# Kernel optimization log

Measured on AMD Instinct MI355X. Metric: run time of the kernel, lower is better.

## Reference

```python
import jax, jax.numpy as jnp
import numpy as np

B, S, E, H = 1, 2048, 1024, 16
D = E // H  # head_dim = 64


def setup_inputs() -> dict:
    key = jax.random.key(0)
    ks = jax.random.split(key, 9)
    sd = 0.02
    hidden_states = jax.random.normal(ks[0], (B, S, E), dtype=jnp.float32)
    # causal mask: positions with mask==0 are filled with -inf (per masked_fill_)
    mask = jnp.tril(jnp.ones((1, 1, S, S), dtype=bool))
    Wq = jax.random.normal(ks[1], (E, E), dtype=jnp.float32) * sd
    bq = jax.random.normal(ks[2], (E,), dtype=jnp.float32) * sd
    Wk = jax.random.normal(ks[3], (D, E), dtype=jnp.float32) * sd
    bk = jax.random.normal(ks[4], (D,), dtype=jnp.float32) * sd
    Wv = jax.random.normal(ks[5], (D, E), dtype=jnp.float32) * sd
    bv = jax.random.normal(ks[6], (D,), dtype=jnp.float32) * sd
    Wo = jax.random.normal(ks[7], (E, E), dtype=jnp.float32) * sd
    bo = jax.random.normal(ks[8], (E,), dtype=jnp.float32) * sd
    return {"hidden_states": hidden_states, "mask": mask,
            "Wq": Wq, "bq": bq, "Wk": Wk, "bk": bk,
            "Wv": Wv, "bv": bv, "Wo": Wo, "bo": bo}


def reference(hidden_states, mask, Wq, bq, Wk, bk, Wv, bv, Wo, bo):
    bsz, tgt_len, embed_dim = hidden_states.shape
    # projections (torch Linear: x @ W^T + b)
    q = hidden_states @ Wq.T + bq                       # [B, S, E]
    q = q.reshape(bsz, tgt_len, H, D).transpose(0, 2, 1, 3)  # [B, H, S, D]
    k = hidden_states @ Wk.T + bk                       # [B, S, D] shared single KV head
    v = hidden_states @ Wv.T + bv                       # [B, S, D]
    scaling = jnp.sqrt(jnp.asarray(D, dtype=hidden_states.dtype))
    # QK^T with implicit broadcast of the shared K head (instead of expand)
    scores = jnp.einsum('bhqd,bkd->bhqk', q, k) / scaling   # [B, H, S, S]
    scores = jnp.where(mask, scores, -jnp.inf)
    probs = jax.nn.softmax(scores, axis=-1)             # dropout p=0 -> identity
    attn = jnp.einsum('bhqk,bkd->bhqd', probs, v)       # [B, H, S, D]
    attn = attn.transpose(0, 2, 1, 3).reshape(bsz, tgt_len, H * D)
    return attn @ Wo.T + bo                             # [B, S, E]
```

## Files before the change

kernel.cpp:

```cpp
#include <hip/hip_runtime.h>
#include <hip/hip_bf16.h>

typedef __hip_bfloat16 bf16;
typedef __attribute__((ext_vector_type(8))) short short8;
typedef __attribute__((ext_vector_type(4))) float f32x4;

__device__ __forceinline__ short8 ld8(const void* p) { return *(const short8*)p; }

__device__ __forceinline__ void async_cp16(bf16* lds, const bf16* g) {
    __builtin_amdgcn_global_load_lds(
        (const __attribute__((address_space(1))) unsigned int*)g,
        (__attribute__((address_space(3))) unsigned int*)lds, 16, 0, 0);
}

struct bf4 { bf16 a, b, c, d; };

__global__ void cast_kernel(const float* __restrict__ s0, bf16* __restrict__ d0, int n0_,
                            const float* __restrict__ s1, bf16* __restrict__ d1, int n1_,
                            const float* __restrict__ s2, bf16* __restrict__ d2, int n2_,
                            const float* __restrict__ s3, bf16* __restrict__ d3, int n3_,
                            const float* __restrict__ s4, bf16* __restrict__ d4, int n4_) {
    const float* srcs[5] = {s0, s1, s2, s3, s4};
    bf16* dsts[5] = {d0, d1, d2, d3, d4};
    int ns[5] = {n0_, n1_, n2_, n3_, n4_};
    int stride = gridDim.x * blockDim.x;
    int t0 = blockIdx.x * blockDim.x + threadIdx.x;
#pragma unroll
    for (int a = 0; a < 5; ++a) {
        const float4* src = (const float4*)srcs[a];
        bf4* dst = (bf4*)dsts[a];
        int n4 = ns[a] >> 2;
        for (int i = t0; i < n4; i += stride) {
            float4 v = src[i];
            bf4 o = {__float2bfloat16(v.x), __float2bfloat16(v.y),
                     __float2bfloat16(v.z), __float2bfloat16(v.w)};
            dst[i] = o;
        }
    }
}

#define GEMM_STAGE(dst, src_base, row0, ldk)                                   \
    _Pragma("unroll")                                                          \
    for (int u = 0; u < 4; ++u) {                                              \
        int t = wave * 4 + u;                                                  \
        int row = t * 4 + (lane >> 4);                                         \
        int gsrc = (lane & 15) ^ (row & 15);                                   \
        async_cp16(&dst[t * 4][0], src_base + (size_t)(row0 + row) * ldk + k0 + gsrc * 8); \
    }

__global__ void qkv_proj_kernel(const bf16* __restrict__ A,
                                const bf16* __restrict__ Wq, const bf16* __restrict__ Wk,
                                const bf16* __restrict__ Wv,
                                const float* __restrict__ bq, const float* __restrict__ bk,
                                const float* __restrict__ bv,
                                bf16* __restrict__ qo, bf16* __restrict__ ko,
                                bf16* __restrict__ vto, int M, int K) {
    __shared__ __align__(16) bf16 As[64][128];
    __shared__ __align__(16) bf16 Bs[64][128];
    const int nt = blockIdx.x;
    const bf16* W;
    const float* bias;
    int mode, nw0;
    if (nt < 16)      { W = Wq; bias = bq; mode = 0; nw0 = nt * 64; }
    else if (nt == 16){ W = Wk; bias = bk; mode = 1; nw0 = 0; }
    else              { W = Wv; bias = bv; mode = 2; nw0 = 0; }

    const int tid = threadIdx.x;
    const int wave = tid >> 6, lane = tid & 63;
    const int l16 = lane & 15, quad = lane >> 4;
    const int m0 = blockIdx.y * 64;

    f32x4 acc[4];
    const f32x4 z = {0.f, 0.f, 0.f, 0.f};
#pragma unroll
    for (int ni = 0; ni < 4; ++ni) acc[ni] = z;

    for (int k0 = 0; k0 < K; k0 += 128) {
        GEMM_STAGE(As, A, m0, K)
        GEMM_STAGE(Bs, W, nw0, K)
        __syncthreads();

        short8 af[4], bfr[4][4];
        {
            int R = wave * 16 + l16;
#pragma unroll
            for (int kc = 0; kc < 4; ++kc)
                af[kc] = ld8(&As[R][((kc * 4 + quad) ^ (R & 15)) * 8]);
        }
#pragma unroll
        for (int ni = 0; ni < 4; ++ni) {
            int r = ni * 16 + l16;
#pragma unroll
            for (int kc = 0; kc < 4; ++kc)
                bfr[kc][ni] = ld8(&Bs[r][((kc * 4 + quad) ^ (r & 15)) * 8]);
        }
#pragma unroll
        for (int kc = 0; kc < 4; ++kc)
#pragma unroll
            for (int ni = 0; ni < 4; ++ni)
                acc[ni] = __builtin_amdgcn_mfma_f32_16x16x32_bf16(
                    af[kc], bfr[kc][ni], acc[ni], 0, 0, 0);
        __syncthreads();
    }

#pragma unroll
    for (int ni = 0; ni < 4; ++ni)
#pragma unroll
        for (int r = 0; r < 4; ++r) {
            int row = m0 + wave * 16 + quad * 4 + r;
            int col = ni * 16 + l16;
            float v = acc[ni][r] + bias[nw0 + col];
            if (mode == 0)
                qo[(size_t)row * 1024 + nt * 64 + col] = __float2bfloat16(v * 0.125f);
            else if (mode == 1)
                ko[(size_t)row * 64 + col] = __float2bfloat16(v);
            else
                vto[(size_t)col * M + row] = __float2bfloat16(v);
        }
}

__global__ void gemm_bt_mfma(const bf16* __restrict__ A, const bf16* __restrict__ W,
                             const float* __restrict__ bias, float* __restrict__ C,
                             int M, int N, int K) {
    __shared__ __align__(16) bf16 As[64][128];
    __shared__ __align__(16) bf16 Bs[64][128];
    const int tid = threadIdx.x;
    const int wave = tid >> 6, lane = tid & 63;
    const int l16 = lane & 15, quad = lane >> 4;
    const int m0 = blockIdx.y * 64, n0 = blockIdx.x * 64;

    f32x4 acc[4];
    const f32x4 z = {0.f, 0.f, 0.f, 0.f};
#pragma unroll
    for (int ni = 0; ni < 4; ++ni) acc[ni] = z;

    for (int k0 = 0; k0 < K; k0 += 128) {
        GEMM_STAGE(As, A, m0, K)
        GEMM_STAGE(Bs, W, n0, K)
        __syncthreads();

        short8 af[4], bfr[4][4];
        {
            int R = wave * 16 + l16;
#pragma unroll
            for (int kc = 0; kc < 4; ++kc)
                af[kc] = ld8(&As[R][((kc * 4 + quad) ^ (R & 15)) * 8]);
        }
#pragma unroll
        for (int ni = 0; ni < 4; ++ni) {
            int r = ni * 16 + l16;
#pragma unroll
            for (int kc = 0; kc < 4; ++kc)
                bfr[kc][ni] = ld8(&Bs[r][((kc * 4 + quad) ^ (r & 15)) * 8]);
        }
#pragma unroll
        for (int kc = 0; kc < 4; ++kc)
#pragma unroll
            for (int ni = 0; ni < 4; ++ni)
                acc[ni] = __builtin_amdgcn_mfma_f32_16x16x32_bf16(
                    af[kc], bfr[kc][ni], acc[ni], 0, 0, 0);
        __syncthreads();
    }

#pragma unroll
    for (int ni = 0; ni < 4; ++ni)
#pragma unroll
        for (int r = 0; r < 4; ++r) {
            int row = m0 + wave * 16 + quad * 4 + r;
            int col = n0 + ni * 16 + l16;
            C[(size_t)row * N + col] = acc[ni][r] + bias[col];
        }
}

__global__ void flash_mfma_kernel(const bf16* __restrict__ Q, const bf16* __restrict__ Kg,
                                  const bf16* __restrict__ VT,
                                  bf16* __restrict__ Opart, float* __restrict__ Lpart,
                                  int S) {
    const int s = blockIdx.x;
    const int c = (s >= 32) ? 1 : 0;
    const int i = (c == 0) ? s : s - 16;

    __shared__ __align__(16) bf16 Ks[2][64][64];
    __shared__ __align__(16) bf16 Vt[2][64][64];
    __shared__ bf16 Ps[4][16][68];

    const int h = blockIdx.y;
    const int q0 = i * 64;
    const int tid = threadIdx.x;
    const int wave = tid >> 6, lane = tid & 63;
    const int l16 = lane & 15, quad = lane >> 4;
    const int lr = lane >> 3, lsw = (lane & 7) ^ (lr & 7);
    const int qrow = q0 + wave * 16;

    short8 qf[2];
#pragma unroll
    for (int kc = 0; kc < 2; ++kc)
        qf[kc] = ld8(Q + (size_t)(qrow + l16) * 1024 + h * 64 + kc * 32 + quad * 8);

    short8 onesf;
    {
        short o = (l16 == 0) ? (short)0x3F80 : (short)0;
        onesf[0]=o; onesf[1]=o; onesf[2]=o; onesf[3]=o;
        onesf[4]=o; onesf[5]=o; onesf[6]=o; onesf[7]=o;
    }

    f32x4 of[4];
    const f32x4 z = {0.f, 0.f, 0.f, 0.f};
#pragma unroll
    for (int dt = 0; dt < 4; ++dt) of[dt] = z;
    f32x4 lacc = z;

    const int jt0 = c * 16;
    const int jt1 = min(c * 16 + 16, i + 1);

    {
        const int j0 = jt0 * 64;
#pragma unroll
        for (int u = 0; u < 2; ++u) {
            int t = wave * 2 + u;
            async_cp16(&Ks[0][t * 8][0], Kg + (size_t)(j0 + t * 8 + lr) * 64 + lsw * 8);
            async_cp16(&Vt[0][t * 8][0], VT + (size_t)(t * 8 + lr) * S + j0 + lsw * 8);
        }
    }

    int buf = 0;
    for (int jt = jt0; jt < jt1; ++jt, buf ^= 1) {
        __syncthreads();
        if (jt + 1 < jt1) {
            const int j0n = (jt + 1) * 64;
#pragma unroll
            for (int u = 0; u < 2; ++u) {
                int t = wave * 2 + u;
                async_cp16(&Ks[buf ^ 1][t * 8][0], Kg + (size_t)(j0n + t * 8 + lr) * 64 + lsw * 8);
                async_cp16(&Vt[buf ^ 1][t * 8][0], VT + (size_t)(t * 8 + lr) * S + j0n + lsw * 8);
            }
        }
        const int j0 = jt * 64;

        f32x4 sc[4];
#pragma unroll
        for (int nt = 0; nt < 4; ++nt) {
            int R = nt * 16 + l16;
            sc[nt] = __builtin_amdgcn_mfma_f32_16x16x32_bf16(
                qf[0], ld8(&Ks[buf][R][(quad ^ (R & 7)) * 8]), z, 0, 0, 0);
            sc[nt] = __builtin_amdgcn_mfma_f32_16x16x32_bf16(
                qf[1], ld8(&Ks[buf][R][((4 + quad) ^ (R & 7)) * 8]), sc[nt], 0, 0, 0);
        }
        bool need_mask = (j0 + 63 > qrow);
        if (need_mask) {
#pragma unroll
            for (int nt = 0; nt < 4; ++nt)
#pragma unroll
                for (int r = 0; r < 4; ++r)
                    if (j0 + nt * 16 + l16 > qrow + quad * 4 + r) sc[nt][r] = -1e30f;
        }

#pragma unroll
        for (int nt = 0; nt < 4; ++nt)
#pragma unroll
            for (int r = 0; r < 4; ++r)
                Ps[wave][quad * 4 + r][nt * 16 + l16] = __float2bfloat16(__expf(sc[nt][r]));

        short8 pf[2];
        pf[0] = ld8(&Ps[wave][l16][quad * 8]);
        pf[1] = ld8(&Ps[wave][l16][32 + quad * 8]);

        lacc = __builtin_amdgcn_mfma_f32_16x16x32_bf16(pf[0], onesf, lacc, 0, 0, 0);
        lacc = __builtin_amdgcn_mfma_f32_16x16x32_bf16(pf[1], onesf, lacc, 0, 0, 0);

#pragma unroll
        for (int dt = 0; dt < 4; ++dt) {
            int R = dt * 16 + l16;
            of[dt] = __builtin_amdgcn_mfma_f32_16x16x32_bf16(
                pf[0], ld8(&Vt[buf][R][(quad ^ (R & 7)) * 8]), of[dt], 0, 0, 0);
            of[dt] = __builtin_amdgcn_mfma_f32_16x16x32_bf16(
                pf[1], ld8(&Vt[buf][R][((4 + quad) ^ (R & 7)) * 8]), of[dt], 0, 0, 0);
        }
    }

    bf16* Op = Opart + ((size_t)s * 16 + h) * 4096;
#pragma unroll
    for (int dt = 0; dt < 4; ++dt)
#pragma unroll
        for (int r = 0; r < 4; ++r) {
            int row = wave * 16 + quad * 4 + r;
            Op[row * 64 + dt * 16 + l16] = __float2bfloat16(of[dt][r]);
        }
    if (l16 == 0) {
        float* L = Lpart + ((size_t)s * 16 + h) * 64;
#pragma unroll
        for (int r = 0; r < 4; ++r)
            L[wave * 16 + quad * 4 + r] = lacc[r];
    }
}

__global__ void flash_merge_kernel(const bf16* __restrict__ Opart,
                                   const float* __restrict__ Lpart,
                                   bf16* __restrict__ attn) {
    const int i = blockIdx.x, h = blockIdx.y;
    const int nch = (i >> 4) + 1;
    const int tid = threadIdx.x;
    const int row = tid >> 2, cg = (tid & 3) * 16;

    float L = 0.f;
    for (int cc = 0; cc < nch; ++cc) {
        int s = (cc == 0) ? i : 16 + i;
        L += Lpart[((size_t)s * 16 + h) * 64 + row];
    }
    float inv = 1.f / L;

    float o[16];
#pragma unroll
    for (int j = 0; j < 16; ++j) o[j] = 0.f;
    for (int cc = 0; cc < nch; ++cc) {
        int s = (cc == 0) ? i : 16 + i;
        const bf16* Op = Opart + ((size_t)s * 16 + h) * 4096 + row * 64 + cg;
#pragma unroll
        for (int j = 0; j < 16; ++j) o[j] += __bfloat162float(Op[j]);
    }
    bf16* dst = attn + (size_t)(i * 64 + row) * 1024 + h * 64 + cg;
#pragma unroll
    for (int j = 0; j < 16; ++j) dst[j] = __float2bfloat16(o[j] * inv);
}

extern "C" void kernel_launch(void* const* d_in, const int* in_sizes, int n_in,
                              void* d_out, int out_size, void* d_ws, size_t ws_size,
                              hipStream_t stream) {
    const int S = 2048, E = 1024, D = 64;

    const float* hs = (const float*)d_in[0];
    const float* Wq = (const float*)d_in[2];
    const float* bq = (const float*)d_in[3];
    const float* Wk = (const float*)d_in[4];
    const float* bk = (const float*)d_in[5];
    const float* Wv = (const float*)d_in[6];
    const float* bv = (const float*)d_in[7];
    const float* Wo = (const float*)d_in[8];
    const float* bo = (const float*)d_in[9];
    float* out = (float*)d_out;

    bf16* ws = (bf16*)d_ws;
    bf16* hsb = ws;
    bf16* wqb = hsb + (size_t)S * E;
    bf16* wkb = wqb + (size_t)E * E;
    bf16* wvb = wkb + (size_t)D * E;
    bf16* wob = wvb + (size_t)D * E;
    bf16* q = wob + (size_t)E * E;
    bf16* kbuf = q + (size_t)S * E;
    bf16* vt = kbuf + (size_t)S * D;
    bf16* attn = vt + (size_t)S * D;
    bf16* Opart = attn + (size_t)S * E;
    float* Lpart = (float*)(Opart + (size_t)768 * 4096);

    dim3 blk(256);
    cast_kernel<<<512, blk, 0, stream>>>(hs, hsb, S * E,
                                         Wq, wqb, E * E,
                                         Wk, wkb, D * E,
                                         Wv, wvb, D * E,
                                         Wo, wob, E * E);
    qkv_proj_kernel<<<dim3(18, S / 64), blk, 0, stream>>>(hsb, wqb, wkb, wvb,
                                                          bq, bk, bv,
                                                          q, kbuf, vt, S, E);
    flash_mfma_kernel<<<dim3(48, 16), blk, 0, stream>>>(q, kbuf, vt, Opart, Lpart, S);
    flash_merge_kernel<<<dim3(32, 16), blk, 0, stream>>>(Opart, Lpart, attn);
    gemm_bt_mfma<<<dim3(E / 64, S / 64), blk, 0, stream>>>(attn, wob, bo, out, S, E, E);
}
```

Baseline: 152.2 us.

## Double-buffer GEMM LDS tiles and split flash KV range into 8-tile chunks

Both the QKV projection and the output GEMM now keep two LDS stages per operand. The next K-tile is prefetched asynchronously while MFMAs run on the current one, and one of the two barriers per iteration is dropped. Separately, the flash split-KV partitioning goes from chunks of 16 KV tiles (48 blocks per head) to chunks of 8 (80 blocks per head), and the merge kernel and workspace offsets are updated to match. This gives more parallelism and better load balance across CUs, at the cost of more partial outputs to write and merge, and double the LDS per GEMM block, which may reduce occupancy.

```diff
diff --git a/kernel.cpp b/kernel.cpp
--- a/kernel.cpp
+++ b/kernel.cpp
@@ -39,13 +39,28 @@
     }
 }
 
-#define GEMM_STAGE(dst, src_base, row0, ldk)                                   \
+#define GEMM_STAGE(dst, src_base, row0, ldk, kk)                               \
     _Pragma("unroll")                                                          \
     for (int u = 0; u < 4; ++u) {                                              \
         int t = wave * 4 + u;                                                  \
         int row = t * 4 + (lane >> 4);                                         \
         int gsrc = (lane & 15) ^ (row & 15);                                   \
-        async_cp16(&dst[t * 4][0], src_base + (size_t)(row0 + row) * ldk + k0 + gsrc * 8); \
+        async_cp16(&dst[t * 4][0], src_base + (size_t)(row0 + row) * ldk + (kk) + gsrc * 8); \
+    }
+
+#define GEMM_FRAGS(buf_a, buf_b)                                               \
+    {                                                                          \
+        int R = wave * 16 + l16;                                               \
+        _Pragma("unroll")                                                      \
+        for (int kc = 0; kc < 4; ++kc)                                         \
+            af[kc] = ld8(&buf_a[R][((kc * 4 + quad) ^ (R & 15)) * 8]);         \
+    }                                                                          \
+    _Pragma("unroll")                                                          \
+    for (int ni = 0; ni < 4; ++ni) {                                           \
+        int r = ni * 16 + l16;                                                 \
+        _Pragma("unroll")                                                      \
+        for (int kc = 0; kc < 4; ++kc)                                         \
+            bfr[kc][ni] = ld8(&buf_b[r][((kc * 4 + quad) ^ (r & 15)) * 8]);    \
     }
 
 __global__ void qkv_proj_kernel(const bf16* __restrict__ A,
@@ -55,8 +70,8 @@
                                 const float* __restrict__ bv,
                                 bf16* __restrict__ qo, bf16* __restrict__ ko,
                                 bf16* __restrict__ vto, int M, int K) {
-    __shared__ __align__(16) bf16 As[64][128];
-    __shared__ __align__(16) bf16 Bs[64][128];
+    __shared__ __align__(16) bf16 As[2][64][128];
+    __shared__ __align__(16) bf16 Bs[2][64][128];
     const int nt = blockIdx.x;
     const bf16* W;
     const float* bias;
@@ -75,32 +90,23 @@
 #pragma unroll
     for (int ni = 0; ni < 4; ++ni) acc[ni] = z;
 
-    for (int k0 = 0; k0 < K; k0 += 128) {
-        GEMM_STAGE(As, A, m0, K)
-        GEMM_STAGE(Bs, W, nw0, K)
+    GEMM_STAGE(As[0], A, m0, K, 0)
+    GEMM_STAGE(Bs[0], W, nw0, K, 0)
+    int buf = 0;
+    for (int k0 = 0; k0 < K; k0 += 128, buf ^= 1) {
         __syncthreads();
-
+        if (k0 + 128 < K) {
+            GEMM_STAGE(As[buf ^ 1], A, m0, K, k0 + 128)
+            GEMM_STAGE(Bs[buf ^ 1], W, nw0, K, k0 + 128)
+        }
         short8 af[4], bfr[4][4];
-        {
-            int R = wave * 16 + l16;
-#pragma unroll
-            for (int kc = 0; kc < 4; ++kc)
-                af[kc] = ld8(&As[R][((kc * 4 + quad) ^ (R & 15)) * 8]);
-        }
-#pragma unroll
-        for (int ni = 0; ni < 4; ++ni) {
-            int r = ni * 16 + l16;
-#pragma unroll
-            for (int kc = 0; kc < 4; ++kc)
-                bfr[kc][ni] = ld8(&Bs[r][((kc * 4 + quad) ^ (r & 15)) * 8]);
-        }
+        GEMM_FRAGS(As[buf], Bs[buf])
 #pragma unroll
         for (int kc = 0; kc < 4; ++kc)
 #pragma unroll
             for (int ni = 0; ni < 4; ++ni)
                 acc[ni] = __builtin_amdgcn_mfma_f32_16x16x32_bf16(
                     af[kc], bfr[kc][ni], acc[ni], 0, 0, 0);
-        __syncthreads();
     }
 
 #pragma unroll
@@ -122,8 +128,8 @@
 __global__ void gemm_bt_mfma(const bf16* __restrict__ A, const bf16* __restrict__ W,
                              const float* __restrict__ bias, float* __restrict__ C,
                              int M, int N, int K) {
-    __shared__ __align__(16) bf16 As[64][128];
-    __shared__ __align__(16) bf16 Bs[64][128];
+    __shared__ __align__(16) bf16 As[2][64][128];
+    __shared__ __align__(16) bf16 Bs[2][64][128];
     const int tid = threadIdx.x;
     const int wave = tid >> 6, lane = tid & 63;
     const int l16 = lane & 15, quad = lane >> 4;
@@ -134,32 +140,23 @@
 #pragma unroll
     for (int ni = 0; ni < 4; ++ni) acc[ni] = z;
 
-    for (int k0 = 0; k0 < K; k0 += 128) {
-        GEMM_STAGE(As, A, m0, K)
-        GEMM_STAGE(Bs, W, n0, K)
+    GEMM_STAGE(As[0], A, m0, K, 0)
+    GEMM_STAGE(Bs[0], W, n0, K, 0)
+    int buf = 0;
+    for (int k0 = 0; k0 < K; k0 += 128, buf ^= 1) {
         __syncthreads();
-
+        if (k0 + 128 < K) {
+            GEMM_STAGE(As[buf ^ 1], A, m0, K, k0 + 128)
+            GEMM_STAGE(Bs[buf ^ 1], W, n0, K, k0 + 128)
+        }
         short8 af[4], bfr[4][4];
-        {
-            int R = wave * 16 + l16;
-#pragma unroll
-            for (int kc = 0; kc < 4; ++kc)
-                af[kc] = ld8(&As[R][((kc * 4 + quad) ^ (R & 15)) * 8]);
-        }
-#pragma unroll
-        for (int ni = 0; ni < 4; ++ni) {
-            int r = ni * 16 + l16;
-#pragma unroll
-            for (int kc = 0; kc < 4; ++kc)
-                bfr[kc][ni] = ld8(&Bs[r][((kc * 4 + quad) ^ (r & 15)) * 8]);
-        }
+        GEMM_FRAGS(As[buf], Bs[buf])
 #pragma unroll
         for (int kc = 0; kc < 4; ++kc)
 #pragma unroll
             for (int ni = 0; ni < 4; ++ni)
                 acc[ni] = __builtin_amdgcn_mfma_f32_16x16x32_bf16(
                     af[kc], bfr[kc][ni], acc[ni], 0, 0, 0);
-        __syncthreads();
     }
 
 #pragma unroll
@@ -177,8 +174,11 @@
                                   bf16* __restrict__ Opart, float* __restrict__ Lpart,
                                   int S) {
     const int s = blockIdx.x;
-    const int c = (s >= 32) ? 1 : 0;
-    const int i = (c == 0) ? s : s - 16;
+    int i, c;
+    if (s < 32)      { c = 0; i = s; }
+    else if (s < 56) { c = 1; i = s - 24; }
+    else if (s < 72) { c = 2; i = s - 40; }
+    else             { c = 3; i = s - 48; }
 
     __shared__ __align__(16) bf16 Ks[2][64][64];
     __shared__ __align__(16) bf16 Vt[2][64][64];
@@ -210,8 +210,8 @@
     for (int dt = 0; dt < 4; ++dt) of[dt] = z;
     f32x4 lacc = z;
 
-    const int jt0 = c * 16;
-    const int jt1 = min(c * 16 + 16, i + 1);
+    const int jt0 = c * 8;
+    const int jt1 = min(c * 8 + 8, i + 1);
 
     {
         const int j0 = jt0 * 64;
@@ -298,13 +298,13 @@
                                    const float* __restrict__ Lpart,
                                    bf16* __restrict__ attn) {
     const int i = blockIdx.x, h = blockIdx.y;
-    const int nch = (i >> 4) + 1;
+    const int nch = (i >> 3) + 1;
     const int tid = threadIdx.x;
     const int row = tid >> 2, cg = (tid & 3) * 16;
 
     float L = 0.f;
     for (int cc = 0; cc < nch; ++cc) {
-        int s = (cc == 0) ? i : 16 + i;
+        int s = (cc == 0) ? i : (cc == 1) ? 24 + i : (cc == 2) ? 40 + i : 48 + i;
         L += Lpart[((size_t)s * 16 + h) * 64 + row];
     }
     float inv = 1.f / L;
@@ -313,7 +313,7 @@
 #pragma unroll
     for (int j = 0; j < 16; ++j) o[j] = 0.f;
     for (int cc = 0; cc < nch; ++cc) {
-        int s = (cc == 0) ? i : 16 + i;
+        int s = (cc == 0) ? i : (cc == 1) ? 24 + i : (cc == 2) ? 40 + i : 48 + i;
         const bf16* Op = Opart + ((size_t)s * 16 + h) * 4096 + row * 64 + cg;
 #pragma unroll
         for (int j = 0; j < 16; ++j) o[j] += __bfloat162float(Op[j]);
@@ -350,7 +350,7 @@
     bf16* vt = kbuf + (size_t)S * D;
     bf16* attn = vt + (size_t)S * D;
     bf16* Opart = attn + (size_t)S * E;
-    float* Lpart = (float*)(Opart + (size_t)768 * 4096);
+    float* Lpart = (float*)(Opart + (size_t)1280 * 4096);
 
     dim3 blk(256);
     cast_kernel<<<512, blk, 0, stream>>>(hs, hsb, S * E,
@@ -361,7 +361,7 @@
     qkv_proj_kernel<<<dim3(18, S / 64), blk, 0, stream>>>(hsb, wqb, wkb, wvb,
                                                           bq, bk, bv,
                                                           q, kbuf, vt, S, E);
-    flash_mfma_kernel<<<dim3(48, 16), blk, 0, stream>>>(q, kbuf, vt, Opart, Lpart, S);
+    flash_mfma_kernel<<<dim3(80, 16), blk, 0, stream>>>(q, kbuf, vt, Opart, Lpart, S);
     flash_merge_kernel<<<dim3(32, 16), blk, 0, stream>>>(Opart, Lpart, attn);
     gemm_bt_mfma<<<dim3(E / 64, S / 64), blk, 0, stream>>>(attn, wob, bo, out, S, E, E);
 }
```

Result: slower. 155.4 us (+2.1%).

## Split causal attention KV range into 8-tile chunks and drop double buffering

Applied to the files above, without the earlier changes.

The causal flash-attention kernel now splits each query tile's key range into chunks of 8 KV tiles instead of 16, for up to four partial chunks per row block. The grid grows from 48 to 80 blocks per head and the merge kernel sums up to four partials. The K/V LDS double buffer becomes a single buffer with a sync before and after each tile. This shortens the longest block's serial work and balances the causal triangle better, at the cost of losing load/compute overlap and adding more partial-output traffic and merge work.

```diff
diff --git a/kernel.cpp b/kernel.cpp
--- a/kernel.cpp
+++ b/kernel.cpp
@@ -177,11 +177,14 @@
                                   bf16* __restrict__ Opart, float* __restrict__ Lpart,
                                   int S) {
     const int s = blockIdx.x;
-    const int c = (s >= 32) ? 1 : 0;
-    const int i = (c == 0) ? s : s - 16;
-
-    __shared__ __align__(16) bf16 Ks[2][64][64];
-    __shared__ __align__(16) bf16 Vt[2][64][64];
+    int i, c;
+    if (s < 32)      { c = 0; i = s; }
+    else if (s < 56) { c = 1; i = s - 24; }
+    else if (s < 72) { c = 2; i = s - 40; }
+    else             { c = 3; i = s - 48; }
+
+    __shared__ __align__(16) bf16 Ks[64][64];
+    __shared__ __align__(16) bf16 Vt[64][64];
     __shared__ bf16 Ps[4][16][68];
 
     const int h = blockIdx.y;
@@ -210,41 +213,27 @@
     for (int dt = 0; dt < 4; ++dt) of[dt] = z;
     f32x4 lacc = z;
 
-    const int jt0 = c * 16;
-    const int jt1 = min(c * 16 + 16, i + 1);
-
-    {
-        const int j0 = jt0 * 64;
+    const int jt0 = c * 8;
+    const int jt1 = min(c * 8 + 8, i + 1);
+
+    for (int jt = jt0; jt < jt1; ++jt) {
+        const int j0 = jt * 64;
 #pragma unroll
         for (int u = 0; u < 2; ++u) {
             int t = wave * 2 + u;
-            async_cp16(&Ks[0][t * 8][0], Kg + (size_t)(j0 + t * 8 + lr) * 64 + lsw * 8);
-            async_cp16(&Vt[0][t * 8][0], VT + (size_t)(t * 8 + lr) * S + j0 + lsw * 8);
-        }
-    }
-
-    int buf = 0;
-    for (int jt = jt0; jt < jt1; ++jt, buf ^= 1) {
-        __syncthreads();
-        if (jt + 1 < jt1) {
-            const int j0n = (jt + 1) * 64;
-#pragma unroll
-            for (int u = 0; u < 2; ++u) {
-                int t = wave * 2 + u;
-                async_cp16(&Ks[buf ^ 1][t * 8][0], Kg + (size_t)(j0n + t * 8 + lr) * 64 + lsw * 8);
-                async_cp16(&Vt[buf ^ 1][t * 8][0], VT + (size_t)(t * 8 + lr) * S + j0n + lsw * 8);
-            }
-        }
-        const int j0 = jt * 64;
+            async_cp16(&Ks[t * 8][0], Kg + (size_t)(j0 + t * 8 + lr) * 64 + lsw * 8);
+            async_cp16(&Vt[t * 8][0], VT + (size_t)(t * 8 + lr) * S + j0 + lsw * 8);
+        }
+        __syncthreads();
 
         f32x4 sc[4];
 #pragma unroll
         for (int nt = 0; nt < 4; ++nt) {
             int R = nt * 16 + l16;
             sc[nt] = __builtin_amdgcn_mfma_f32_16x16x32_bf16(
-                qf[0], ld8(&Ks[buf][R][(quad ^ (R & 7)) * 8]), z, 0, 0, 0);
+                qf[0], ld8(&Ks[R][(quad ^ (R & 7)) * 8]), z, 0, 0, 0);
             sc[nt] = __builtin_amdgcn_mfma_f32_16x16x32_bf16(
-                qf[1], ld8(&Ks[buf][R][((4 + quad) ^ (R & 7)) * 8]), sc[nt], 0, 0, 0);
+                qf[1], ld8(&Ks[R][((4 + quad) ^ (R & 7)) * 8]), sc[nt], 0, 0, 0);
         }
         bool need_mask = (j0 + 63 > qrow);
         if (need_mask) {
@@ -272,10 +261,11 @@
         for (int dt = 0; dt < 4; ++dt) {
             int R = dt * 16 + l16;
             of[dt] = __builtin_amdgcn_mfma_f32_16x16x32_bf16(
-                pf[0], ld8(&Vt[buf][R][(quad ^ (R & 7)) * 8]), of[dt], 0, 0, 0);
+                pf[0], ld8(&Vt[R][(quad ^ (R & 7)) * 8]), of[dt], 0, 0, 0);
             of[dt] = __builtin_amdgcn_mfma_f32_16x16x32_bf16(
-                pf[1], ld8(&Vt[buf][R][((4 + quad) ^ (R & 7)) * 8]), of[dt], 0, 0, 0);
-        }
+                pf[1], ld8(&Vt[R][((4 + quad) ^ (R & 7)) * 8]), of[dt], 0, 0, 0);
+        }
+        __syncthreads();
     }
 
     bf16* Op = Opart + ((size_t)s * 16 + h) * 4096;
@@ -298,13 +288,13 @@
                                    const float* __restrict__ Lpart,
                                    bf16* __restrict__ attn) {
     const int i = blockIdx.x, h = blockIdx.y;
-    const int nch = (i >> 4) + 1;
+    const int nch = (i >> 3) + 1;
     const int tid = threadIdx.x;
     const int row = tid >> 2, cg = (tid & 3) * 16;
 
     float L = 0.f;
     for (int cc = 0; cc < nch; ++cc) {
-        int s = (cc == 0) ? i : 16 + i;
+        int s = (cc == 0) ? i : (cc == 1) ? 24 + i : (cc == 2) ? 40 + i : 48 + i;
         L += Lpart[((size_t)s * 16 + h) * 64 + row];
     }
     float inv = 1.f / L;
@@ -313,7 +303,7 @@
 #pragma unroll
     for (int j = 0; j < 16; ++j) o[j] = 0.f;
     for (int cc = 0; cc < nch; ++cc) {
-        int s = (cc == 0) ? i : 16 + i;
+        int s = (cc == 0) ? i : (cc == 1) ? 24 + i : (cc == 2) ? 40 + i : 48 + i;
         const bf16* Op = Opart + ((size_t)s * 16 + h) * 4096 + row * 64 + cg;
 #pragma unroll
         for (int j = 0; j < 16; ++j) o[j] += __bfloat162float(Op[j]);
@@ -350,7 +340,7 @@
     bf16* vt = kbuf + (size_t)S * D;
     bf16* attn = vt + (size_t)S * D;
     bf16* Opart = attn + (size_t)S * E;
-    float* Lpart = (float*)(Opart + (size_t)768 * 4096);
+    float* Lpart = (float*)(Opart + (size_t)1280 * 4096);
 
     dim3 blk(256);
     cast_kernel<<<512, blk, 0, stream>>>(hs, hsb, S * E,
@@ -361,7 +351,7 @@
     qkv_proj_kernel<<<dim3(18, S / 64), blk, 0, stream>>>(hsb, wqb, wkb, wvb,
                                                           bq, bk, bv,
                                                           q, kbuf, vt, S, E);
-    flash_mfma_kernel<<<dim3(48, 16), blk, 0, stream>>>(q, kbuf, vt, Opart, Lpart, S);
+    flash_mfma_kernel<<<dim3(80, 16), blk, 0, stream>>>(q, kbuf, vt, Opart, Lpart, S);
     flash_merge_kernel<<<dim3(32, 16), blk, 0, stream>>>(Opart, Lpart, attn);
     gemm_bt_mfma<<<dim3(E / 64, S / 64), blk, 0, stream>>>(attn, wob, bo, out, S, E, E);
 }
```

After: 146.5 us. 3.8% less time.
